# Kernel optimization log

Measured on AMD Instinct MI355X. Metric: run time of the kernel, lower is better.

Reference implementation:

```python
import jax, jax.numpy as jnp
import numpy as np
import math

H = 16
D_MODEL = 1024
B, S = 2, 2048

def setup_inputs() -> dict:
    key = jax.random.key(0)
    ks = jax.random.split(key, 7)
    q = jax.random.normal(ks[0], (B, S, D_MODEL), dtype=jnp.float32)
    k = jax.random.normal(ks[1], (B, S, D_MODEL), dtype=jnp.float32)
    v = jax.random.normal(ks[2], (B, S, D_MODEL), dtype=jnp.float32)
    mask = jnp.ones((1, 1, S, S), dtype=jnp.int32)
    sc = 1.0 / math.sqrt(D_MODEL)
    W_Q = jax.random.normal(ks[3], (D_MODEL, D_MODEL), dtype=jnp.float32) * sc
    W_K = jax.random.normal(ks[4], (D_MODEL, D_MODEL), dtype=jnp.float32) * sc
    W_V = jax.random.normal(ks[5], (D_MODEL, D_MODEL), dtype=jnp.float32) * sc
    W_T = jax.random.normal(ks[6], (D_MODEL, D_MODEL), dtype=jnp.float32) * sc
    return {"q": q, "k": k, "v": v, "mask": mask, "W_Q": W_Q, "W_K": W_K, "W_V": W_V, "W_T": W_T}

def reference(q, k, v, mask, W_Q, W_K, W_V, W_T):
    # W matrices stored as (in, out); nn.Linear applies x @ W.T with W (out,in),
    # equivalent here since we treat these directly as projection matrices.
    def split_heads(x):  # [B,S,D] -> [B,H,S,hd]
        Bq, Sq, Dq = x.shape
        return x.reshape(Bq, Sq, H, Dq // H).transpose(0, 2, 1, 3)

    Q = split_heads(q @ W_Q)
    K = split_heads(k @ W_K)
    V = split_heads(v @ W_V)
    d_k = Q.shape[-1]
    score = jnp.einsum("bhqd,bhkd->bhqk", Q, K) / math.sqrt(d_k)
    score = jnp.where(mask == 0, jnp.float32(-1e9), score)
    attn = jax.nn.softmax(score, axis=-1)
    out = jnp.einsum("bhqk,bhkd->bhqd", attn, V)
    out = out.transpose(0, 2, 1, 3).reshape(q.shape[0], q.shape[1], D_MODEL)
    return out @ W_T
```

## Files before the change

kernel.cpp:

```cpp
#include <hip/hip_runtime.h>
#include <hip/hip_bf16.h>
#include <stdint.h>

#define H  16
#define DM 1024
#define BB 2
#define SS 2048
#define HD 64

#define QSCALE 0.18033688011112042f
#define MASKVAL -57.7078f

typedef __attribute__((ext_vector_type(8))) short bf16x8;
typedef __attribute__((ext_vector_type(4))) float f32x4;

__device__ __forceinline__ short f2bf(float f) {
  __hip_bfloat16 h = __float2bfloat16(f);
  return *reinterpret_cast<short*>(&h);
}

__device__ __forceinline__ unsigned pack_bf16(float a, float b) {
#if __has_builtin(__builtin_amdgcn_cvt_pk_bf16_f32)
  typedef __attribute__((ext_vector_type(2))) __bf16 bf16x2_t;
  bf16x2_t p = __builtin_amdgcn_cvt_pk_bf16_f32(a, b);
  unsigned u;
  __builtin_memcpy(&u, &p, 4);
  return u;
#else
  unsigned ua = __builtin_bit_cast(unsigned, a);
  unsigned ub = __builtin_bit_cast(unsigned, b);
  ua = (ua + 0x7FFFu + ((ua >> 16) & 1u)) >> 16;
  ub = (ub + 0x7FFFu + ((ub >> 16) & 1u));
  return (ub & 0xFFFF0000u) | ua;
#endif
}

__device__ __forceinline__ void load16_lds(const short* g, short* l) {
  __builtin_amdgcn_global_load_lds(
      (const __attribute__((address_space(1))) void*)g,
      (__attribute__((address_space(3))) void*)l, 16, 0, 0);
}

__global__ void prep_kernel(const float* __restrict__ Wq, const float* __restrict__ Wk,
                            const float* __restrict__ Wv, const float* __restrict__ Wt,
                            short* __restrict__ WTall,
                            const float* __restrict__ q, const float* __restrict__ k,
                            const float* __restrict__ v, short* __restrict__ Abf,
                            const int4* __restrict__ mask4, int* __restrict__ flag) {
  int z = blockIdx.z;
  int t = threadIdx.x;
  if (z < 4) {
    if (blockIdx.x >= 1024) return;
    __shared__ short tile[32][33];
    const float* src = (z == 0) ? Wq : (z == 1) ? Wk : (z == 2) ? Wv : Wt;
    short* out = WTall + (size_t)z * DM * DM;
    int c0 = (blockIdx.x & 31) * 32, r0 = (blockIdx.x >> 5) * 32;
    int tx = t & 31, ty = t >> 5;
    for (int j = 0; j < 4; j++)
      tile[ty + j * 8][tx] = f2bf(src[(size_t)(r0 + ty + j * 8) * DM + c0 + tx]);
    __syncthreads();
    for (int j = 0; j < 4; j++)
      out[(size_t)(c0 + ty + j * 8) * DM + r0 + tx] = tile[tx][ty + j * 8];
  } else if (z < 7) {
    int zz = z - 4;
    const float* src = (zz == 0) ? q : (zz == 1) ? k : v;
    short* out = Abf + (size_t)zz * BB * SS * DM;
    size_t i = ((size_t)blockIdx.x * 256 + t) * 4;
    float4 f = *(const float4*)&src[i];
    uint2 p = {pack_bf16(f.x, f.y), pack_bf16(f.z, f.w)};
    *(uint2*)&out[i] = p;
  } else {
    int idx = blockIdx.x * 256 + t;
    int4 m = mask4[idx];
    if (m.x == 0 || m.y == 0 || m.z == 0 || m.w == 0) atomicOr(flag, 1);
  }
}

__global__ void transpose_w_kernel(const float* __restrict__ Wq, const float* __restrict__ Wk,
                                   const float* __restrict__ Wv, const float* __restrict__ Wt,
                                   short* __restrict__ dst, int* __restrict__ flag) {
  if (blockIdx.x == 0 && blockIdx.y == 0 && blockIdx.z == 0 &&
      threadIdx.y == 0 && threadIdx.x < 2) flag[threadIdx.x] = 0;
  __shared__ short tile[32][33];
  int z = blockIdx.z;
  const float* src = (z == 0) ? Wq : (z == 1) ? Wk : (z == 2) ? Wv : Wt;
  short* out = dst + (size_t)z * DM * DM;
  int c0 = blockIdx.x * 32, r0 = blockIdx.y * 32;
  int tx = threadIdx.x, ty = threadIdx.y;
  for (int j = 0; j < 4; j++)
    tile[ty + j * 8][tx] = f2bf(src[(size_t)(r0 + ty + j * 8) * DM + c0 + tx]);
  __syncthreads();
  for (int j = 0; j < 4; j++)
    out[(size_t)(c0 + ty + j * 8) * DM + r0 + tx] = tile[tx][ty + j * 8];
}

__global__ void mask_scan_kernel(const int4* __restrict__ mask4, int n4, int* __restrict__ flag) {
  int idx = blockIdx.x * blockDim.x + threadIdx.x;
  int stride = gridDim.x * blockDim.x;
  int any = 0;
  for (int i = idx; i < n4; i += stride) {
    int4 m = mask4[i];
    if (m.x == 0 || m.y == 0 || m.z == 0 || m.w == 0) any = 1;
  }
  if (any) atomicOr(flag, 1);
}

__global__ void flag_init_kernel(int* flag) { if (threadIdx.x < 2) flag[threadIdx.x] = 0; }

__global__ void transpose_v_kernel(const short* __restrict__ Vbuf, short* __restrict__ Vt) {
  __shared__ short tile[32][33];
  int bh = blockIdx.z;
  int s0 = blockIdx.x * 32, d0 = blockIdx.y * 32;
  int tx = threadIdx.x, ty = threadIdx.y;
  for (int j = 0; j < 4; j++)
    tile[ty + j * 8][tx] = Vbuf[((size_t)bh * SS + s0 + ty + j * 8) * HD + d0 + tx];
  __syncthreads();
  for (int j = 0; j < 4; j++)
    Vt[((size_t)bh * HD + d0 + ty + j * 8) * SS + s0 + tx] = tile[tx][ty + j * 8];
}

__global__ void signal_fill_kernel(float* __restrict__ out, int n) {
  int i = blockIdx.x * blockDim.x + threadIdx.x;
  if (i < n) out[i] = 1.0f;
}

template <int AF32>
__device__ __forceinline__ void gemm_fast_body(const void* __restrict__ Av,
                                               const short* __restrict__ Bt,
                                               void* __restrict__ Cv, int mode, float scale) {
  __shared__ __align__(16) short As[128 * 32];
  __shared__ __align__(16) short Bs[128 * 32];
  int m0 = blockIdx.x * 128, n0 = blockIdx.y * 128;
  int t = threadIdx.x;
  int lane = t & 63, w = t >> 6;
  int l16 = lane & 15, quad = lane >> 4;
  int wm = (w >> 1) * 64, wn = (w & 1) * 64;
  f32x4 acc[4][4] = {};

  for (int k0 = 0; k0 < DM; k0 += 32) {
    if (AF32) {
      const float* A = (const float*)Av;
      for (int i = 0; i < 4; i++) {
        int c = t + i * 256;
        int row = c >> 3, seg = c & 7;
        float4 f = *(const float4*)&A[(size_t)(m0 + row) * DM + k0 + seg * 4];
        uint2 p = {pack_bf16(f.x, f.y), pack_bf16(f.z, f.w)};
        *(uint2*)&As[row * 32 + seg * 4] = p;
      }
    } else {
      const short* A = (const short*)Av;
      for (int i = 0; i < 2; i++) {
        int c = t + i * 256;
        load16_lds(&A[(size_t)(m0 + (c >> 2)) * DM + k0 + (c & 3) * 8], &As[c * 8]);
      }
    }
    for (int i = 0; i < 2; i++) {
      int c = t + i * 256;
      load16_lds(&Bt[(size_t)(n0 + (c >> 2)) * DM + k0 + (c & 3) * 8], &Bs[c * 8]);
    }
    __syncthreads();
    bf16x8 af[4], bfr[4];
    for (int i = 0; i < 4; i++) af[i]  = *(const bf16x8*)&As[(wm + i * 16 + l16) * 32 + quad * 8];
    for (int i = 0; i < 4; i++) bfr[i] = *(const bf16x8*)&Bs[(wn + i * 16 + l16) * 32 + quad * 8];
    for (int mi = 0; mi < 4; mi++)
      for (int ni = 0; ni < 4; ni++)
        acc[mi][ni] = __builtin_amdgcn_mfma_f32_16x16x32_bf16(af[mi], bfr[ni], acc[mi][ni], 0, 0, 0);
    __syncthreads();
  }

  for (int mi = 0; mi < 4; mi++)
    for (int ni = 0; ni < 4; ni++)
      for (int r = 0; r < 4; r++) {
        int m = m0 + wm + mi * 16 + quad * 4 + r;
        int n = n0 + wn + ni * 16 + l16;
        if (mode == 0) {
          short* C = (short*)Cv;
          int b = m >> 11, s = m & (SS - 1);
          int h = n >> 6, d = n & (HD - 1);
          C[(((size_t)(b * H + h) * SS) + s) * HD + d] = f2bf(acc[mi][ni][r] * scale);
        } else {
          float* C = (float*)Cv;
          C[(size_t)m * DM + n] = acc[mi][ni][r];
        }
      }
}

template <int AF32>
__global__ __launch_bounds__(256, 2) void gemm_qkv_fast_kernel(
    const void* __restrict__ A0, const void* __restrict__ A1, const void* __restrict__ A2,
    const short* __restrict__ WTall,
    short* __restrict__ Qb, short* __restrict__ Kb, short* __restrict__ Vb) {
  int z = blockIdx.z;
  const void* A = (z == 0) ? A0 : (z == 1) ? A1 : A2;
  const short* B = WTall + (size_t)z * DM * DM;
  short* C = (z == 0) ? Qb : (z == 1) ? Kb : Vb;
  gemm_fast_body<AF32>(A, B, (void*)C, 0, (z == 0) ? QSCALE : 1.0f);
}

__global__ __launch_bounds__(256, 2) void gemm_out_fast_kernel(
    const short* __restrict__ Obuf, const short* __restrict__ WtT, float* __restrict__ out) {
  gemm_fast_body<0>((const void*)Obuf, WtT, (void*)out, 2, 1.0f);
}

#define LDT 40
#define LDB 136

template <int AF32>
__device__ __forceinline__ void gemm_legacy_body(const void* __restrict__ Av,
                                                 const float* __restrict__ Bm,
                                                 void* __restrict__ Cv, int mode, float scale) {
  __shared__ __align__(16) short As[128 * LDT];
  __shared__ __align__(16) short Bsh[32 * LDB];
  int m0 = blockIdx.x * 128, n0 = blockIdx.y * 128;
  int t = threadIdx.x;
  int lane = t & 63, w = t >> 6;
  int l16 = lane & 15, quad = lane >> 4;
  int wm = (w >> 1) * 64, wn = (w & 1) * 64;
  f32x4 acc[4][4] = {};

  for (int k0 = 0; k0 < DM; k0 += 32) {
    if (AF32) {
      const float* A = (const float*)Av;
      for (int i = 0; i < 4; i++) {
        int c = t + i * 256;
        int row = c >> 3, seg = c & 7;
        float4 f = *(const float4*)&A[(size_t)(m0 + row) * DM + k0 + seg * 4];
        uint2 p = {pack_bf16(f.x, f.y), pack_bf16(f.z, f.w)};
        *(uint2*)&As[row * LDT + seg * 4] = p;
      }
    } else {
      const short* A = (const short*)Av;
      for (int i = 0; i < 2; i++) {
        int c = t + i * 256;
        int row = c >> 2, seg = c & 3;
        *(int4*)&As[row * LDT + seg * 8] = *(const int4*)&A[(size_t)(m0 + row) * DM + k0 + seg * 8];
      }
    }
    for (int i = 0; i < 4; i++) {
      int c = t + i * 256;
      int krow = c >> 5, nseg = c & 31;
      float4 f = *(const float4*)&Bm[(size_t)(k0 + krow) * DM + n0 + nseg * 4];
      uint2 p = {pack_bf16(f.x, f.y), pack_bf16(f.z, f.w)};
      *(uint2*)&Bsh[krow * LDB + nseg * 4] = p;
    }
    __syncthreads();
    bf16x8 af[4], bfr[4];
    for (int i = 0; i < 4; i++) af[i] = *(const bf16x8*)&As[(wm + i * 16 + l16) * LDT + quad * 8];
    for (int i = 0; i < 4; i++) {
      bf16x8 tmp;
      for (int j = 0; j < 8; j++) tmp[j] = Bsh[(quad * 8 + j) * LDB + wn + i * 16 + l16];
      bfr[i] = tmp;
    }
    for (int mi = 0; mi < 4; mi++)
      for (int ni = 0; ni < 4; ni++)
        acc[mi][ni] = __builtin_amdgcn_mfma_f32_16x16x32_bf16(af[mi], bfr[ni], acc[mi][ni], 0, 0, 0);
    __syncthreads();
  }

  for (int mi = 0; mi < 4; mi++)
    for (int ni = 0; ni < 4; ni++)
      for (int r = 0; r < 4; r++) {
        int m = m0 + wm + mi * 16 + quad * 4 + r;
        int n = n0 + wn + ni * 16 + l16;
        if (mode == 0) {
          short* C = (short*)Cv;
          int b = m >> 11, s = m & (SS - 1);
          int h = n >> 6, d = n & (HD - 1);
          C[(((size_t)(b * H + h) * SS) + s) * HD + d] = f2bf(acc[mi][ni][r] * scale);
        } else {
          float* C = (float*)Cv;
          C[(size_t)m * DM + n] = acc[mi][ni][r];
        }
      }
}

__global__ __launch_bounds__(256, 2) void gemm_qkv_legacy_kernel(
    const float* __restrict__ q, const float* __restrict__ k, const float* __restrict__ v,
    const float* __restrict__ B0, const float* __restrict__ B1, const float* __restrict__ B2,
    short* __restrict__ Qb, short* __restrict__ Kb, short* __restrict__ Vb) {
  int z = blockIdx.z;
  const float* A = (z == 0) ? q : (z == 1) ? k : v;
  const float* B = (z == 0) ? B0 : (z == 1) ? B1 : B2;
  short* C = (z == 0) ? Qb : (z == 1) ? Kb : Vb;
  gemm_legacy_body<1>((const void*)A, B, (void*)C, 0, (z == 0) ? QSCALE : 1.0f);
}

__global__ __launch_bounds__(256, 2) void gemm_out_legacy_kernel(
    const short* __restrict__ Obuf, const float* __restrict__ Wt, float* __restrict__ out) {
  gemm_legacy_body<0>((const void*)Obuf, Wt, (void*)out, 2, 1.0f);
}

#define LDP 72

__global__ __launch_bounds__(256, 2) void attn128_kernel(
    const short* __restrict__ Q, const short* __restrict__ K,
    const short* __restrict__ Vt, const int* __restrict__ mask,
    const int* __restrict__ flag, short* __restrict__ O) {
  __shared__ __align__(16) short Ks[64 * 64];
  __shared__ __align__(16) short Vs[64 * 64];
  __shared__ __align__(16) short Ps[4][32 * LDP];

  int bh = blockIdx.y;
  int q0 = blockIdx.x * 128;
  int t = threadIdx.x, lane = t & 63, w = t >> 6;
  int l16 = lane & 15, quad = lane >> 4;
  int use_mask = flag[0];

  bf16x8 aq[2][2];
  for (int g = 0; g < 2; g++) {
    const short* qrow = Q + ((size_t)bh * SS + q0 + w * 32 + g * 16 + l16) * HD;
    aq[g][0] = *(const bf16x8*)&qrow[quad * 8];
    aq[g][1] = *(const bf16x8*)&qrow[32 + quad * 8];
  }

  float lsum[2] = {0.f, 0.f};
  f32x4 oacc[2][4] = {};

  const short* Kbase = K  + (size_t)bh * SS * HD;
  const short* Vbase = Vt + (size_t)bh * HD * SS;

  for (int kt = 0; kt < SS / 64; kt++) {
    int kb = kt * 64;
    for (int i = 0; i < 2; i++) {
      int p = t + i * 256;
      int rp = p >> 3, cp = p & 7;
      int lc = cp ^ (rp & 7);
      load16_lds(&Kbase[(size_t)(kb + rp) * HD + lc * 8], &Ks[p * 8]);
      load16_lds(&Vbase[(size_t)rp * SS + kb + lc * 8], &Vs[p * 8]);
    }
    __syncthreads();

    if (!use_mask) {
      for (int kb2 = 0; kb2 < 4; kb2++) {
        int krow = kb2 * 16 + l16;
        bf16x8 k0 = *(const bf16x8*)&Ks[krow * 64 + ((quad ^ (l16 & 7)) * 8)];
        bf16x8 k1 = *(const bf16x8*)&Ks[krow * 64 + (((quad + 4) ^ (l16 & 7)) * 8)];
        for (int g = 0; g < 2; g++) {
          f32x4 sc = {};
          sc = __builtin_amdgcn_mfma_f32_16x16x32_bf16(k0, aq[g][0], sc, 0, 0, 0);
          sc = __builtin_amdgcn_mfma_f32_16x16x32_bf16(k1, aq[g][1], sc, 0, 0, 0);
          float p0 = __builtin_exp2f(sc[0]);
          float p1 = __builtin_exp2f(sc[1]);
          float p2 = __builtin_exp2f(sc[2]);
          float p3 = __builtin_exp2f(sc[3]);
          lsum[g] += (p0 + p1) + (p2 + p3);
          uint2 packed = {pack_bf16(p0, p1), pack_bf16(p2, p3)};
          *(uint2*)&Ps[w][(g * 16 + l16) * LDP + kb2 * 16 + quad * 4] = packed;
        }
      }
    } else {
      for (int kb2 = 0; kb2 < 4; kb2++) {
        int krow = kb2 * 16 + l16;
        bf16x8 k0 = *(const bf16x8*)&Ks[krow * 64 + ((quad ^ (l16 & 7)) * 8)];
        bf16x8 k1 = *(const bf16x8*)&Ks[krow * 64 + (((quad + 4) ^ (l16 & 7)) * 8)];
        for (int g = 0; g < 2; g++) {
          f32x4 sc = {};
          sc = __builtin_amdgcn_mfma_f32_16x16x32_bf16(k0, aq[g][0], sc, 0, 0, 0);
          sc = __builtin_amdgcn_mfma_f32_16x16x32_bf16(k1, aq[g][1], sc, 0, 0, 0);
          int qg = q0 + w * 32 + g * 16 + l16;
          for (int r = 0; r < 4; r++) {
            int kg = kb + kb2 * 16 + quad * 4 + r;
            if (mask[(size_t)qg * SS + kg] == 0) sc[r] = MASKVAL;
          }
          float p0 = __builtin_exp2f(sc[0]);
          float p1 = __builtin_exp2f(sc[1]);
          float p2 = __builtin_exp2f(sc[2]);
          float p3 = __builtin_exp2f(sc[3]);
          lsum[g] += (p0 + p1) + (p2 + p3);
          uint2 packed = {pack_bf16(p0, p1), pack_bf16(p2, p3)};
          *(uint2*)&Ps[w][(g * 16 + l16) * LDP + kb2 * 16 + quad * 4] = packed;
        }
      }
    }

    for (int c = 0; c < 2; c++) {
      bf16x8 ap[2];
      for (int g = 0; g < 2; g++)
        ap[g] = *(const bf16x8*)&Ps[w][(g * 16 + l16) * LDP + c * 32 + quad * 8];
      for (int nb2 = 0; nb2 < 4; nb2++) {
        bf16x8 bv = *(const bf16x8*)&Vs[(nb2 * 16 + l16) * 64 + (((c * 4 + quad) ^ (l16 & 7)) * 8)];
        for (int g = 0; g < 2; g++)
          oacc[g][nb2] = __builtin_amdgcn_mfma_f32_16x16x32_bf16(ap[g], bv, oacc[g][nb2], 0, 0, 0);
      }
    }
    __syncthreads();
  }

  for (int g = 0; g < 2; g++) {
    lsum[g] += __shfl_xor(lsum[g], 16);
    lsum[g] += __shfl_xor(lsum[g], 32);
  }

  int b = bh >> 4, h = bh & 15;
  for (int g = 0; g < 2; g++)
    for (int r = 0; r < 4; r++) {
      float inv = 1.0f / __shfl(lsum[g], quad * 4 + r);
      int qg = q0 + w * 32 + g * 16 + quad * 4 + r;
      for (int nb2 = 0; nb2 < 4; nb2++) {
        int d = nb2 * 16 + l16;
        O[((size_t)(b * SS + qg)) * DM + h * HD + d] = f2bf(oacc[g][nb2][r] * inv);
      }
    }
}

__global__ __launch_bounds__(256, 4) void attn64_kernel(
    const short* __restrict__ Q, const short* __restrict__ K,
    const short* __restrict__ V, const int* __restrict__ mask,
    const int* __restrict__ flag, short* __restrict__ O) {
  __shared__ __align__(16) short Ks[64 * 64];
  __shared__ __align__(16) short Vs[64 * 64];
  __shared__ __align__(16) short Ps[4][16 * LDP];

  int bh = blockIdx.y;
  int q0 = blockIdx.x * 64;
  int t = threadIdx.x, lane = t & 63, w = t >> 6;
  int l16 = lane & 15, quad = lane >> 4;
  int use_mask = flag[0];

  const short* qrow = Q + ((size_t)bh * SS + q0 + w * 16 + l16) * HD;
  bf16x8 aq0 = *(const bf16x8*)&qrow[quad * 8];
  bf16x8 aq1 = *(const bf16x8*)&qrow[32 + quad * 8];

  float lsum[4] = {0.f, 0.f, 0.f, 0.f};
  f32x4 oacc[4] = {};

  const short* Kbase = K + (size_t)bh * SS * HD;
  const short* Vbase = V + (size_t)bh * SS * HD;
  int dd = t & 63, h2 = t >> 6;

  for (int kt = 0; kt < SS / 64; kt++) {
    int kb = kt * 64;
    for (int i = 0; i < 2; i++) {
      int p = t + i * 256;
      int rp = p >> 3, cp = p & 7;
      int lc = cp ^ (rp & 7);
      load16_lds(&Kbase[(size_t)(kb + rp) * HD + lc * 8], &Ks[p * 8]);
    }
    for (int sgi = 0; sgi < 2; sgi++) {
      int sg = h2 * 2 + sgi;
      short tmp[8];
      for (int jj = 0; jj < 8; jj++)
        tmp[jj] = Vbase[(size_t)(kb + sg * 8 + jj) * HD + dd];
      *(int4*)&Vs[dd * 64 + ((sg ^ (dd & 7)) * 8)] = *(const int4*)tmp;
    }
    __syncthreads();

    for (int nb = 0; nb < 4; nb++) {
      f32x4 sc = {};
      bf16x8 bk0 = *(const bf16x8*)&Ks[(nb * 16 + l16) * 64 + ((quad ^ (l16 & 7)) * 8)];
      bf16x8 bk1 = *(const bf16x8*)&Ks[(nb * 16 + l16) * 64 + (((quad + 4) ^ (l16 & 7)) * 8)];
      sc = __builtin_amdgcn_mfma_f32_16x16x32_bf16(aq0, bk0, sc, 0, 0, 0);
      sc = __builtin_amdgcn_mfma_f32_16x16x32_bf16(aq1, bk1, sc, 0, 0, 0);
      if (use_mask) {
        int kg = kb + nb * 16 + l16;
        for (int r = 0; r < 4; r++) {
          int qg = q0 + w * 16 + quad * 4 + r;
          if (mask[(size_t)qg * SS + kg] == 0) sc[r] = MASKVAL;
        }
      }
      for (int r = 0; r < 4; r++) {
        float pv = __builtin_exp2f(sc[r]);
        lsum[r] += pv;
        Ps[w][(quad * 4 + r) * LDP + nb * 16 + l16] = f2bf(pv);
      }
    }

    for (int c = 0; c < 2; c++) {
      bf16x8 ap = *(const bf16x8*)&Ps[w][l16 * LDP + c * 32 + quad * 8];
      for (int nb2 = 0; nb2 < 4; nb2++) {
        bf16x8 bv = *(const bf16x8*)&Vs[(nb2 * 16 + l16) * 64 + (((c * 4 + quad) ^ (l16 & 7)) * 8)];
        oacc[nb2] = __builtin_amdgcn_mfma_f32_16x16x32_bf16(ap, bv, oacc[nb2], 0, 0, 0);
      }
    }
    __syncthreads();
  }

  for (int st = 1; st < 16; st <<= 1)
    for (int r = 0; r < 4; r++) lsum[r] += __shfl_xor(lsum[r], st);

  int b = bh >> 4, h = bh & 15;
  for (int r = 0; r < 4; r++) {
    float inv = 1.0f / lsum[r];
    int qg = q0 + w * 16 + quad * 4 + r;
    for (int nb2 = 0; nb2 < 4; nb2++) {
      int d = nb2 * 16 + l16;
      O[((size_t)(b * SS + qg)) * DM + h * HD + d] = f2bf(oacc[nb2][r] * inv);
    }
  }
}

extern "C" void kernel_launch(void* const* d_in, const int* in_sizes, int n_in,
                              void* d_out, int out_size, void* d_ws, size_t ws_size,
                              hipStream_t stream) {
  const float* q    = (const float*)d_in[0];
  const float* k    = (const float*)d_in[1];
  const float* v    = (const float*)d_in[2];
  const int*   mask = (const int*)d_in[3];
  const float* Wq   = (const float*)d_in[4];
  const float* Wk   = (const float*)d_in[5];
  const float* Wv   = (const float*)d_in[6];
  const float* Wt   = (const float*)d_in[7];
  float* out = (float*)d_out;

  char* ws = (char*)d_ws;
  const size_t MB = 1024ull * 1024ull;
  const size_t NEED_A = 66 * MB;
  const size_t NEED_B = 40 * MB + 4096;
  const size_t NEED_C = 32 * MB + 4096;

  if (ws_size >= NEED_A) {
    short* WTall = (short*)(ws);
    short* Qbuf  = (short*)(ws + 8 * MB);
    short* Kbuf  = (short*)(ws + 16 * MB);
    short* Vbuf  = (short*)(ws + 24 * MB);
    short* Obuf  = (short*)(ws + 32 * MB);
    int*   flag  = (int*)(ws + 40 * MB);
    short* Abf   = (short*)(ws + 41 * MB);
    short* Vt    = Abf;

    hipMemsetAsync(flag, 0, 8, stream);
    prep_kernel<<<dim3(4096, 1, 8), 256, 0, stream>>>(
        Wq, Wk, Wv, Wt, WTall, q, k, v, Abf, (const int4*)mask, flag);
    gemm_qkv_fast_kernel<0><<<dim3(BB * SS / 128, DM / 128, 3), 256, 0, stream>>>(
        Abf, Abf + (size_t)BB * SS * DM, Abf + 2ull * BB * SS * DM, WTall, Qbuf, Kbuf, Vbuf);
    transpose_v_kernel<<<dim3(SS / 32, HD / 32, BB * H), dim3(32, 8), 0, stream>>>(Vbuf, Vt);
    attn128_kernel<<<dim3(SS / 128, BB * H), 256, 0, stream>>>(Qbuf, Kbuf, Vt, mask, flag, Obuf);
    gemm_out_fast_kernel<<<dim3(BB * SS / 128, DM / 128), 256, 0, stream>>>(
        Obuf, WTall + 3ull * DM * DM, out);
  } else if (ws_size >= NEED_B) {
    short* WTall = (short*)(ws);
    short* Qbuf  = (short*)(ws + 8 * MB);
    short* Kbuf  = (short*)(ws + 16 * MB);
    short* Vbuf  = (short*)(ws + 24 * MB);
    short* Obuf  = (short*)(ws + 32 * MB);
    int*   flag  = (int*)(ws + 40 * MB);

    transpose_w_kernel<<<dim3(32, 32, 4), dim3(32, 8), 0, stream>>>(Wq, Wk, Wv, Wt, WTall, flag);
    mask_scan_kernel<<<512, 256, 0, stream>>>((const int4*)mask, SS * SS / 4, flag);
    gemm_qkv_fast_kernel<1><<<dim3(BB * SS / 128, DM / 128, 3), 256, 0, stream>>>(
        q, k, v, WTall, Qbuf, Kbuf, Vbuf);
    attn64_kernel<<<dim3(SS / 64, BB * H), 256, 0, stream>>>(Qbuf, Kbuf, Vbuf, mask, flag, Obuf);
    gemm_out_fast_kernel<<<dim3(BB * SS / 128, DM / 128), 256, 0, stream>>>(
        Obuf, WTall + 3ull * DM * DM, out);
  } else if (ws_size >= NEED_C) {
    short* Qbuf = (short*)(ws);
    short* Kbuf = (short*)(ws + 8 * MB);
    short* Vbuf = (short*)(ws + 16 * MB);
    short* Obuf = (short*)(ws + 24 * MB);
    int*   flag = (int*)(ws + 32 * MB);

    flag_init_kernel<<<1, 64, 0, stream>>>(flag);
    mask_scan_kernel<<<512, 256, 0, stream>>>((const int4*)mask, SS * SS / 4, flag);
    gemm_qkv_legacy_kernel<<<dim3(BB * SS / 128, DM / 128, 3), 256, 0, stream>>>(
        q, k, v, Wq, Wk, Wv, Qbuf, Kbuf, Vbuf);
    attn64_kernel<<<dim3(SS / 64, BB * H), 256, 0, stream>>>(Qbuf, Kbuf, Vbuf, mask, flag, Obuf);
    gemm_out_legacy_kernel<<<dim3(BB * SS / 128, DM / 128), 256, 0, stream>>>(Obuf, Wt, out);
  } else {
    signal_fill_kernel<<<(BB * SS * DM + 255) / 256, 256, 0, stream>>>(out, BB * SS * DM);
  }
}
```

Baseline: 260.1 us.

## Double-buffer K/V tiles in attention and use 8 waves of 16 query rows

Restructures the attention kernel to 512 threads, with each wave owning 16 query rows instead of 32. K and V tiles are double-buffered in LDS so the next tile's global-to-LDS load overlaps compute on the current one, leaving a single barrier per iteration. It also raises wave priority around the PV MFMA block. The trade-off is less K/V register reuse per wave and doubled LDS for K/V, which may reduce occupancy.

Measured after the change: 252.6 us. 1.03x faster.

```diff
diff --git a/kernel.cpp b/kernel.cpp
--- a/kernel.cpp
+++ b/kernel.cpp
@@ -292,13 +292,58 @@
 
 #define LDP 72
 
-__global__ __launch_bounds__(256, 2) void attn128_kernel(
+template <int UM>
+__device__ __forceinline__ void attn_tile(
+    const short* __restrict__ Ksb, const short* __restrict__ Vsb,
+    short* __restrict__ Psw, const bf16x8 aq[2], f32x4 oacc[4], float& lsum,
+    const int* __restrict__ mask, int qg, int kb) {
+  int lane = threadIdx.x & 63;
+  int l16 = lane & 15, quad = lane >> 4;
+
+#pragma unroll
+  for (int kb2 = 0; kb2 < 4; kb2++) {
+    int krow = kb2 * 16 + l16;
+    bf16x8 k0 = *(const bf16x8*)&Ksb[krow * 64 + ((quad ^ (l16 & 7)) * 8)];
+    bf16x8 k1 = *(const bf16x8*)&Ksb[krow * 64 + (((quad + 4) ^ (l16 & 7)) * 8)];
+    f32x4 sc = {};
+    sc = __builtin_amdgcn_mfma_f32_16x16x32_bf16(k0, aq[0], sc, 0, 0, 0);
+    sc = __builtin_amdgcn_mfma_f32_16x16x32_bf16(k1, aq[1], sc, 0, 0, 0);
+    if (UM) {
+#pragma unroll
+      for (int r = 0; r < 4; r++) {
+        int kg = kb + kb2 * 16 + quad * 4 + r;
+        if (mask[(size_t)qg * SS + kg] == 0) sc[r] = MASKVAL;
+      }
+    }
+    float p0 = __builtin_exp2f(sc[0]);
+    float p1 = __builtin_exp2f(sc[1]);
+    float p2 = __builtin_exp2f(sc[2]);
+    float p3 = __builtin_exp2f(sc[3]);
+    lsum += (p0 + p1) + (p2 + p3);
+    uint2 packed = {pack_bf16(p0, p1), pack_bf16(p2, p3)};
+    *(uint2*)&Psw[l16 * LDP + kb2 * 16 + quad * 4] = packed;
+  }
+
+  __builtin_amdgcn_s_setprio(1);
+#pragma unroll
+  for (int c = 0; c < 2; c++) {
+    bf16x8 ap = *(const bf16x8*)&Psw[l16 * LDP + c * 32 + quad * 8];
+#pragma unroll
+    for (int nb2 = 0; nb2 < 4; nb2++) {
+      bf16x8 bv = *(const bf16x8*)&Vsb[(nb2 * 16 + l16) * 64 + (((c * 4 + quad) ^ (l16 & 7)) * 8)];
+      oacc[nb2] = __builtin_amdgcn_mfma_f32_16x16x32_bf16(ap, bv, oacc[nb2], 0, 0, 0);
+    }
+  }
+  __builtin_amdgcn_s_setprio(0);
+}
+
+__global__ __launch_bounds__(512, 4) void attn128_kernel(
     const short* __restrict__ Q, const short* __restrict__ K,
     const short* __restrict__ Vt, const int* __restrict__ mask,
     const int* __restrict__ flag, short* __restrict__ O) {
-  __shared__ __align__(16) short Ks[64 * 64];
-  __shared__ __align__(16) short Vs[64 * 64];
-  __shared__ __align__(16) short Ps[4][32 * LDP];
+  __shared__ __align__(16) short Ks[2][64 * 64];
+  __shared__ __align__(16) short Vs[2][64 * 64];
+  __shared__ __align__(16) short Ps[8][16 * LDP];
 
   int bh = blockIdx.y;
   int q0 = blockIdx.x * 128;
@@ -306,101 +351,64 @@
   int l16 = lane & 15, quad = lane >> 4;
   int use_mask = flag[0];
 
-  bf16x8 aq[2][2];
-  for (int g = 0; g < 2; g++) {
-    const short* qrow = Q + ((size_t)bh * SS + q0 + w * 32 + g * 16 + l16) * HD;
-    aq[g][0] = *(const bf16x8*)&qrow[quad * 8];
-    aq[g][1] = *(const bf16x8*)&qrow[32 + quad * 8];
-  }
-
-  float lsum[2] = {0.f, 0.f};
-  f32x4 oacc[2][4] = {};
+  const short* qrow = Q + ((size_t)bh * SS + q0 + w * 16 + l16) * HD;
+  bf16x8 aq[2] = {*(const bf16x8*)&qrow[quad * 8], *(const bf16x8*)&qrow[32 + quad * 8]};
+
+  float lsum = 0.f;
+  f32x4 oacc[4] = {};
 
   const short* Kbase = K  + (size_t)bh * SS * HD;
   const short* Vbase = Vt + (size_t)bh * HD * SS;
 
-  for (int kt = 0; kt < SS / 64; kt++) {
-    int kb = kt * 64;
-    for (int i = 0; i < 2; i++) {
-      int p = t + i * 256;
-      int rp = p >> 3, cp = p & 7;
-      int lc = cp ^ (rp & 7);
-      load16_lds(&Kbase[(size_t)(kb + rp) * HD + lc * 8], &Ks[p * 8]);
-      load16_lds(&Vbase[(size_t)rp * SS + kb + lc * 8], &Vs[p * 8]);
-    }
-    __syncthreads();
-
-    if (!use_mask) {
-      for (int kb2 = 0; kb2 < 4; kb2++) {
-        int krow = kb2 * 16 + l16;
-        bf16x8 k0 = *(const bf16x8*)&Ks[krow * 64 + ((quad ^ (l16 & 7)) * 8)];
-        bf16x8 k1 = *(const bf16x8*)&Ks[krow * 64 + (((quad + 4) ^ (l16 & 7)) * 8)];
-        for (int g = 0; g < 2; g++) {
-          f32x4 sc = {};
-          sc = __builtin_amdgcn_mfma_f32_16x16x32_bf16(k0, aq[g][0], sc, 0, 0, 0);
-          sc = __builtin_amdgcn_mfma_f32_16x16x32_bf16(k1, aq[g][1], sc, 0, 0, 0);
-          float p0 = __builtin_exp2f(sc[0]);
-          float p1 = __builtin_exp2f(sc[1]);
-          float p2 = __builtin_exp2f(sc[2]);
-          float p3 = __builtin_exp2f(sc[3]);
-          lsum[g] += (p0 + p1) + (p2 + p3);
-          uint2 packed = {pack_bf16(p0, p1), pack_bf16(p2, p3)};
-          *(uint2*)&Ps[w][(g * 16 + l16) * LDP + kb2 * 16 + quad * 4] = packed;
-        }
-      }
-    } else {
-      for (int kb2 = 0; kb2 < 4; kb2++) {
-        int krow = kb2 * 16 + l16;
-        bf16x8 k0 = *(const bf16x8*)&Ks[krow * 64 + ((quad ^ (l16 & 7)) * 8)];
-        bf16x8 k1 = *(const bf16x8*)&Ks[krow * 64 + (((quad + 4) ^ (l16 & 7)) * 8)];
-        for (int g = 0; g < 2; g++) {
-          f32x4 sc = {};
-          sc = __builtin_amdgcn_mfma_f32_16x16x32_bf16(k0, aq[g][0], sc, 0, 0, 0);
-          sc = __builtin_amdgcn_mfma_f32_16x16x32_bf16(k1, aq[g][1], sc, 0, 0, 0);
-          int qg = q0 + w * 32 + g * 16 + l16;
-          for (int r = 0; r < 4; r++) {
-            int kg = kb + kb2 * 16 + quad * 4 + r;
-            if (mask[(size_t)qg * SS + kg] == 0) sc[r] = MASKVAL;
-          }
-          float p0 = __builtin_exp2f(sc[0]);
-          float p1 = __builtin_exp2f(sc[1]);
-          float p2 = __builtin_exp2f(sc[2]);
-          float p3 = __builtin_exp2f(sc[3]);
-          lsum[g] += (p0 + p1) + (p2 + p3);
-          uint2 packed = {pack_bf16(p0, p1), pack_bf16(p2, p3)};
-          *(uint2*)&Ps[w][(g * 16 + l16) * LDP + kb2 * 16 + quad * 4] = packed;
-        }
-      }
-    }
-
-    for (int c = 0; c < 2; c++) {
-      bf16x8 ap[2];
-      for (int g = 0; g < 2; g++)
-        ap[g] = *(const bf16x8*)&Ps[w][(g * 16 + l16) * LDP + c * 32 + quad * 8];
-      for (int nb2 = 0; nb2 < 4; nb2++) {
-        bf16x8 bv = *(const bf16x8*)&Vs[(nb2 * 16 + l16) * 64 + (((c * 4 + quad) ^ (l16 & 7)) * 8)];
-        for (int g = 0; g < 2; g++)
-          oacc[g][nb2] = __builtin_amdgcn_mfma_f32_16x16x32_bf16(ap[g], bv, oacc[g][nb2], 0, 0, 0);
-      }
-    }
-    __syncthreads();
-  }
-
-  for (int g = 0; g < 2; g++) {
-    lsum[g] += __shfl_xor(lsum[g], 16);
-    lsum[g] += __shfl_xor(lsum[g], 32);
-  }
+  int rp = t >> 3, lc = (t & 7) ^ (rp & 7);
+  const short* kSrc = &Kbase[(size_t)rp * HD + lc * 8];
+  const short* vSrc = &Vbase[(size_t)rp * SS + lc * 8];
+  int qg = q0 + w * 16 + l16;
+
+  load16_lds(kSrc, &Ks[0][t * 8]);
+  load16_lds(vSrc, &Vs[0][t * 8]);
+  asm volatile("s_waitcnt vmcnt(0)" ::: "memory");
+  __builtin_amdgcn_s_barrier();
+
+  int cur = 0;
+  if (!use_mask) {
+    for (int kt = 0; kt < SS / 64 - 1; kt++) {
+      int kb1 = (kt + 1) * 64;
+      load16_lds(kSrc + (size_t)kb1 * HD, &Ks[cur ^ 1][t * 8]);
+      load16_lds(vSrc + kb1, &Vs[cur ^ 1][t * 8]);
+      attn_tile<0>(Ks[cur], Vs[cur], Ps[w], aq, oacc, lsum, mask, qg, kt * 64);
+      asm volatile("s_waitcnt vmcnt(0)" ::: "memory");
+      __builtin_amdgcn_s_barrier();
+      cur ^= 1;
+    }
+    attn_tile<0>(Ks[cur], Vs[cur], Ps[w], aq, oacc, lsum, mask, qg, SS - 64);
+  } else {
+    for (int kt = 0; kt < SS / 64 - 1; kt++) {
+      int kb1 = (kt + 1) * 64;
+      load16_lds(kSrc + (size_t)kb1 * HD, &Ks[cur ^ 1][t * 8]);
+      load16_lds(vSrc + kb1, &Vs[cur ^ 1][t * 8]);
+      attn_tile<1>(Ks[cur], Vs[cur], Ps[w], aq, oacc, lsum, mask, qg, kt * 64);
+      asm volatile("s_waitcnt vmcnt(0)" ::: "memory");
+      __builtin_amdgcn_s_barrier();
+      cur ^= 1;
+    }
+    attn_tile<1>(Ks[cur], Vs[cur], Ps[w], aq, oacc, lsum, mask, qg, SS - 64);
+  }
+
+  lsum += __shfl_xor(lsum, 16);
+  lsum += __shfl_xor(lsum, 32);
 
   int b = bh >> 4, h = bh & 15;
-  for (int g = 0; g < 2; g++)
-    for (int r = 0; r < 4; r++) {
-      float inv = 1.0f / __shfl(lsum[g], quad * 4 + r);
-      int qg = q0 + w * 32 + g * 16 + quad * 4 + r;
-      for (int nb2 = 0; nb2 < 4; nb2++) {
-        int d = nb2 * 16 + l16;
-        O[((size_t)(b * SS + qg)) * DM + h * HD + d] = f2bf(oacc[g][nb2][r] * inv);
-      }
-    }
+#pragma unroll
+  for (int r = 0; r < 4; r++) {
+    float inv = 1.0f / __shfl(lsum, quad * 4 + r);
+    int qq = q0 + w * 16 + quad * 4 + r;
+#pragma unroll
+    for (int nb2 = 0; nb2 < 4; nb2++) {
+      int d = nb2 * 16 + l16;
+      O[((size_t)(b * SS + qq)) * DM + h * HD + d] = f2bf(oacc[nb2][r] * inv);
+    }
+  }
 }
 
 __global__ __launch_bounds__(256, 4) void attn64_kernel(
@@ -524,7 +532,7 @@
     gemm_qkv_fast_kernel<0><<<dim3(BB * SS / 128, DM / 128, 3), 256, 0, stream>>>(
         Abf, Abf + (size_t)BB * SS * DM, Abf + 2ull * BB * SS * DM, WTall, Qbuf, Kbuf, Vbuf);
     transpose_v_kernel<<<dim3(SS / 32, HD / 32, BB * H), dim3(32, 8), 0, stream>>>(Vbuf, Vt);
-    attn128_kernel<<<dim3(SS / 128, BB * H), 256, 0, stream>>>(Qbuf, Kbuf, Vt, mask, flag, Obuf);
+    attn128_kernel<<<dim3(SS / 128, BB * H), 512, 0, stream>>>(Qbuf, Kbuf, Vt, mask, flag, Obuf);
     gemm_out_fast_kernel<<<dim3(BB * SS / 128, DM / 128), 256, 0, stream>>>(
         Obuf, WTall + 3ull * DM * DM, out);
   } else if (ws_size >= NEED_B) {
```

## Double-buffer K/V tiles in attn128 and remap block indices

Applied to the files above, without the earlier changes.

The attention kernel now keeps two LDS buffers for K and V. The next tile's global-to-LDS loads are issued before the current tile is computed, and each iteration waits on a single barrier instead of two. The per-tile work moves into a templated helper that raises wave priority around the PV MFMAs, and the loops are fully unrolled. Block indices are remapped so that neighbouring workgroups take different heads and query tiles, which may change cache locality. In exchange, LDS use per block doubles for K and V, which could affect occupancy.

Result: no change. 257.7 us (-0.9%).

```diff
diff --git a/kernel.cpp b/kernel.cpp
--- a/kernel.cpp
+++ b/kernel.cpp
@@ -292,21 +292,79 @@
 
 #define LDP 72
 
+template <int UM>
+__device__ __forceinline__ void attn_tile2(
+    const short* __restrict__ Ksb, const short* __restrict__ Vsb,
+    short* __restrict__ Psw, const bf16x8 aq[2][2], f32x4 oacc[2][4], float lsum[2],
+    const int* __restrict__ mask, int qbase, int kb) {
+  int lane = threadIdx.x & 63;
+  int l16 = lane & 15, quad = lane >> 4;
+
+#pragma unroll
+  for (int kb2 = 0; kb2 < 4; kb2++) {
+    int krow = kb2 * 16 + l16;
+    bf16x8 k0 = *(const bf16x8*)&Ksb[krow * 64 + ((quad ^ (l16 & 7)) * 8)];
+    bf16x8 k1 = *(const bf16x8*)&Ksb[krow * 64 + (((quad + 4) ^ (l16 & 7)) * 8)];
+#pragma unroll
+    for (int g = 0; g < 2; g++) {
+      f32x4 sc = {};
+      sc = __builtin_amdgcn_mfma_f32_16x16x32_bf16(k0, aq[g][0], sc, 0, 0, 0);
+      sc = __builtin_amdgcn_mfma_f32_16x16x32_bf16(k1, aq[g][1], sc, 0, 0, 0);
+      if (UM) {
+        int qg = qbase + g * 16 + l16;
+#pragma unroll
+        for (int r = 0; r < 4; r++) {
+          int kg = kb + kb2 * 16 + quad * 4 + r;
+          if (mask[(size_t)qg * SS + kg] == 0) sc[r] = MASKVAL;
+        }
+      }
+      float p0 = __builtin_exp2f(sc[0]);
+      float p1 = __builtin_exp2f(sc[1]);
+      float p2 = __builtin_exp2f(sc[2]);
+      float p3 = __builtin_exp2f(sc[3]);
+      lsum[g] += (p0 + p1) + (p2 + p3);
+      uint2 packed = {pack_bf16(p0, p1), pack_bf16(p2, p3)};
+      *(uint2*)&Psw[(g * 16 + l16) * LDP + kb2 * 16 + quad * 4] = packed;
+    }
+  }
+
+  __builtin_amdgcn_s_setprio(1);
+#pragma unroll
+  for (int c = 0; c < 2; c++) {
+    bf16x8 ap[2];
+#pragma unroll
+    for (int g = 0; g < 2; g++)
+      ap[g] = *(const bf16x8*)&Psw[(g * 16 + l16) * LDP + c * 32 + quad * 8];
+#pragma unroll
+    for (int nb2 = 0; nb2 < 4; nb2++) {
+      bf16x8 bv = *(const bf16x8*)&Vsb[(nb2 * 16 + l16) * 64 + (((c * 4 + quad) ^ (l16 & 7)) * 8)];
+#pragma unroll
+      for (int g = 0; g < 2; g++)
+        oacc[g][nb2] = __builtin_amdgcn_mfma_f32_16x16x32_bf16(ap[g], bv, oacc[g][nb2], 0, 0, 0);
+    }
+  }
+  __builtin_amdgcn_s_setprio(0);
+}
+
 __global__ __launch_bounds__(256, 2) void attn128_kernel(
     const short* __restrict__ Q, const short* __restrict__ K,
     const short* __restrict__ Vt, const int* __restrict__ mask,
     const int* __restrict__ flag, short* __restrict__ O) {
-  __shared__ __align__(16) short Ks[64 * 64];
-  __shared__ __align__(16) short Vs[64 * 64];
+  __shared__ __align__(16) short Ks[2][64 * 64];
+  __shared__ __align__(16) short Vs[2][64 * 64];
   __shared__ __align__(16) short Ps[4][32 * LDP];
 
-  int bh = blockIdx.y;
-  int q0 = blockIdx.x * 128;
+  int bx = blockIdx.x, by = blockIdx.y;
+  int bh = (bx & 7) * 4 + (by >> 3);
+  int qt = (by & 7) * 2 + (bx >> 3);
+  int q0 = qt * 128;
+
   int t = threadIdx.x, lane = t & 63, w = t >> 6;
   int l16 = lane & 15, quad = lane >> 4;
   int use_mask = flag[0];
 
   bf16x8 aq[2][2];
+#pragma unroll
   for (int g = 0; g < 2; g++) {
     const short* qrow = Q + ((size_t)bh * SS + q0 + w * 32 + g * 16 + l16) * HD;
     aq[g][0] = *(const bf16x8*)&qrow[quad * 8];
@@ -318,84 +376,62 @@
 
   const short* Kbase = K  + (size_t)bh * SS * HD;
   const short* Vbase = Vt + (size_t)bh * HD * SS;
-
-  for (int kt = 0; kt < SS / 64; kt++) {
-    int kb = kt * 64;
-    for (int i = 0; i < 2; i++) {
-      int p = t + i * 256;
-      int rp = p >> 3, cp = p & 7;
-      int lc = cp ^ (rp & 7);
-      load16_lds(&Kbase[(size_t)(kb + rp) * HD + lc * 8], &Ks[p * 8]);
-      load16_lds(&Vbase[(size_t)rp * SS + kb + lc * 8], &Vs[p * 8]);
-    }
-    __syncthreads();
-
-    if (!use_mask) {
-      for (int kb2 = 0; kb2 < 4; kb2++) {
-        int krow = kb2 * 16 + l16;
-        bf16x8 k0 = *(const bf16x8*)&Ks[krow * 64 + ((quad ^ (l16 & 7)) * 8)];
-        bf16x8 k1 = *(const bf16x8*)&Ks[krow * 64 + (((quad + 4) ^ (l16 & 7)) * 8)];
-        for (int g = 0; g < 2; g++) {
-          f32x4 sc = {};
-          sc = __builtin_amdgcn_mfma_f32_16x16x32_bf16(k0, aq[g][0], sc, 0, 0, 0);
-          sc = __builtin_amdgcn_mfma_f32_16x16x32_bf16(k1, aq[g][1], sc, 0, 0, 0);
-          float p0 = __builtin_exp2f(sc[0]);
-          float p1 = __builtin_exp2f(sc[1]);
-          float p2 = __builtin_exp2f(sc[2]);
-          float p3 = __builtin_exp2f(sc[3]);
-          lsum[g] += (p0 + p1) + (p2 + p3);
-          uint2 packed = {pack_bf16(p0, p1), pack_bf16(p2, p3)};
-          *(uint2*)&Ps[w][(g * 16 + l16) * LDP + kb2 * 16 + quad * 4] = packed;
-        }
-      }
-    } else {
-      for (int kb2 = 0; kb2 < 4; kb2++) {
-        int krow = kb2 * 16 + l16;
-        bf16x8 k0 = *(const bf16x8*)&Ks[krow * 64 + ((quad ^ (l16 & 7)) * 8)];
-        bf16x8 k1 = *(const bf16x8*)&Ks[krow * 64 + (((quad + 4) ^ (l16 & 7)) * 8)];
-        for (int g = 0; g < 2; g++) {
-          f32x4 sc = {};
-          sc = __builtin_amdgcn_mfma_f32_16x16x32_bf16(k0, aq[g][0], sc, 0, 0, 0);
-          sc = __builtin_amdgcn_mfma_f32_16x16x32_bf16(k1, aq[g][1], sc, 0, 0, 0);
-          int qg = q0 + w * 32 + g * 16 + l16;
-          for (int r = 0; r < 4; r++) {
-            int kg = kb + kb2 * 16 + quad * 4 + r;
-            if (mask[(size_t)qg * SS + kg] == 0) sc[r] = MASKVAL;
-          }
-          float p0 = __builtin_exp2f(sc[0]);
-          float p1 = __builtin_exp2f(sc[1]);
-          float p2 = __builtin_exp2f(sc[2]);
-          float p3 = __builtin_exp2f(sc[3]);
-          lsum[g] += (p0 + p1) + (p2 + p3);
-          uint2 packed = {pack_bf16(p0, p1), pack_bf16(p2, p3)};
-          *(uint2*)&Ps[w][(g * 16 + l16) * LDP + kb2 * 16 + quad * 4] = packed;
-        }
-      }
-    }
-
-    for (int c = 0; c < 2; c++) {
-      bf16x8 ap[2];
-      for (int g = 0; g < 2; g++)
-        ap[g] = *(const bf16x8*)&Ps[w][(g * 16 + l16) * LDP + c * 32 + quad * 8];
-      for (int nb2 = 0; nb2 < 4; nb2++) {
-        bf16x8 bv = *(const bf16x8*)&Vs[(nb2 * 16 + l16) * 64 + (((c * 4 + quad) ^ (l16 & 7)) * 8)];
-        for (int g = 0; g < 2; g++)
-          oacc[g][nb2] = __builtin_amdgcn_mfma_f32_16x16x32_bf16(ap[g], bv, oacc[g][nb2], 0, 0, 0);
-      }
-    }
-    __syncthreads();
-  }
-
+  int qbase = q0 + w * 32;
+
+  int rp0 = t >> 3, lc0 = (t & 7) ^ (rp0 & 7);
+  int p1 = t + 256;
+  int rp1 = p1 >> 3, lc1 = (p1 & 7) ^ (rp1 & 7);
+
+  load16_lds(&Kbase[(size_t)rp0 * HD + lc0 * 8], &Ks[0][t * 8]);
+  load16_lds(&Kbase[(size_t)rp1 * HD + lc1 * 8], &Ks[0][p1 * 8]);
+  load16_lds(&Vbase[(size_t)rp0 * SS + lc0 * 8], &Vs[0][t * 8]);
+  load16_lds(&Vbase[(size_t)rp1 * SS + lc1 * 8], &Vs[0][p1 * 8]);
+  asm volatile("s_waitcnt vmcnt(0)" ::: "memory");
+  __builtin_amdgcn_s_barrier();
+
+  int cur = 0;
+  if (!use_mask) {
+    for (int kt = 0; kt < SS / 64 - 1; kt++) {
+      int kb1 = (kt + 1) * 64;
+      load16_lds(&Kbase[(size_t)(kb1 + rp0) * HD + lc0 * 8], &Ks[cur ^ 1][t * 8]);
+      load16_lds(&Kbase[(size_t)(kb1 + rp1) * HD + lc1 * 8], &Ks[cur ^ 1][p1 * 8]);
+      load16_lds(&Vbase[(size_t)rp0 * SS + kb1 + lc0 * 8], &Vs[cur ^ 1][t * 8]);
+      load16_lds(&Vbase[(size_t)rp1 * SS + kb1 + lc1 * 8], &Vs[cur ^ 1][p1 * 8]);
+      attn_tile2<0>(Ks[cur], Vs[cur], Ps[w], aq, oacc, lsum, mask, qbase, kt * 64);
+      asm volatile("s_waitcnt vmcnt(0) lgkmcnt(0)" ::: "memory");
+      __builtin_amdgcn_s_barrier();
+      cur ^= 1;
+    }
+    attn_tile2<0>(Ks[cur], Vs[cur], Ps[w], aq, oacc, lsum, mask, qbase, SS - 64);
+  } else {
+    for (int kt = 0; kt < SS / 64 - 1; kt++) {
+      int kb1 = (kt + 1) * 64;
+      load16_lds(&Kbase[(size_t)(kb1 + rp0) * HD + lc0 * 8], &Ks[cur ^ 1][t * 8]);
+      load16_lds(&Kbase[(size_t)(kb1 + rp1) * HD + lc1 * 8], &Ks[cur ^ 1][p1 * 8]);
+      load16_lds(&Vbase[(size_t)rp0 * SS + kb1 + lc0 * 8], &Vs[cur ^ 1][t * 8]);
+      load16_lds(&Vbase[(size_t)rp1 * SS + kb1 + lc1 * 8], &Vs[cur ^ 1][p1 * 8]);
+      attn_tile2<1>(Ks[cur], Vs[cur], Ps[w], aq, oacc, lsum, mask, qbase, kt * 64);
+      asm volatile("s_waitcnt vmcnt(0) lgkmcnt(0)" ::: "memory");
+      __builtin_amdgcn_s_barrier();
+      cur ^= 1;
+    }
+    attn_tile2<1>(Ks[cur], Vs[cur], Ps[w], aq, oacc, lsum, mask, qbase, SS - 64);
+  }
+
+#pragma unroll
   for (int g = 0; g < 2; g++) {
     lsum[g] += __shfl_xor(lsum[g], 16);
     lsum[g] += __shfl_xor(lsum[g], 32);
   }
 
   int b = bh >> 4, h = bh & 15;
+#pragma unroll
   for (int g = 0; g < 2; g++)
+#pragma unroll
     for (int r = 0; r < 4; r++) {
       float inv = 1.0f / __shfl(lsum[g], quad * 4 + r);
       int qg = q0 + w * 32 + g * 16 + quad * 4 + r;
+#pragma unroll
       for (int nb2 = 0; nb2 < 4; nb2++) {
         int d = nb2 * 16 + l16;
         O[((size_t)(b * SS + qg)) * DM + h * HD + d] = f2bf(oacc[g][nb2][r] * inv);
```
